# Kernel tuning notes

Measured on AMD Instinct MI355X. Metric: run time of the kernel, lower is better.

The kernel has to match this reference:

```python
import jax, jax.numpy as jnp
import numpy as np
import math

B, S, D, H = 2, 2048, 1024, 16
DH = D // H

def setup_inputs() -> dict:
    key = jax.random.key(0)
    ks = jax.random.split(key, 12)
    s = 1.0 / math.sqrt(D)
    return {
        "q": jax.random.normal(ks[0], (B, S, D), jnp.float32),
        "k": jax.random.normal(ks[1], (B, S, D), jnp.float32),
        "v": jax.random.normal(ks[2], (B, S, D), jnp.float32),
        "mask": jnp.tril(jnp.ones((S, S), dtype=bool)),  # causal mask
        "Wq": jax.random.normal(ks[3], (D, D), jnp.float32) * s,
        "bq": jnp.zeros((D,), jnp.float32),
        "Wk": jax.random.normal(ks[4], (D, D), jnp.float32) * s,
        "bk": jnp.zeros((D,), jnp.float32),
        "Wv": jax.random.normal(ks[5], (D, D), jnp.float32) * s,
        "bv": jnp.zeros((D,), jnp.float32),
        "Wo": jax.random.normal(ks[6], (D, D), jnp.float32) * s,
        "bo": jnp.zeros((D,), jnp.float32),
    }

def _split_heads(x):
    b, s, _ = x.shape
    return x.reshape(b, s, H, DH).transpose(0, 2, 1, 3)  # [B,H,S,DH]

def reference(q, k, v, mask, Wq, bq, Wk, bk, Wv, bv, Wo, bo):
    qh = _split_heads(q @ Wq.T + bq)
    kh = _split_heads(k @ Wk.T + bk)
    vh = _split_heads(v @ Wv.T + bv)
    scale = 1.0 / math.sqrt(DH)
    scores = jnp.einsum('bhqd,bhkd->bhqk', qh, kh) * scale  # [B,H,S,S]
    scores = jnp.where(mask[None, None, :, :], scores, -jnp.inf)
    attn = jax.nn.softmax(scores, axis=-1)
    out = jnp.einsum('bhqk,bhkd->bhqd', attn, vh)  # [B,H,S,DH]
    out = out.transpose(0, 2, 1, 3).reshape(B, S, D)  # combine heads
    return out @ Wo.T + bo
```

## Files before the change

### kernel.cpp

```cpp
#include <hip/hip_runtime.h>

typedef unsigned int u32;
typedef unsigned short u16;
typedef __attribute__((ext_vector_type(8))) short bf16x8;
typedef __attribute__((ext_vector_type(8))) u16 u16x8;
typedef __attribute__((ext_vector_type(4))) u16 u16x4;
typedef __attribute__((ext_vector_type(4))) float f32x4;
typedef __attribute__((ext_vector_type(2))) u32 u32x2;

#define AS1 __attribute__((address_space(1)))
#define AS3 __attribute__((address_space(3)))

__device__ __forceinline__ void gload_lds16(const void* g, void* l) {
  __builtin_amdgcn_global_load_lds((const AS1 u32*)g, (AS3 u32*)l, 16, 0, 0);
}

__device__ __forceinline__ u16 f2bf(float f) {
  union { float f; u32 u; } x; x.f = f;
  u32 u = x.u;
  return (u16)((u + 0x7fffu + ((u >> 16) & 1u)) >> 16);
}

__device__ __forceinline__ float bf2f(u16 v) {
  union { u32 u; float f; } x; x.u = (u32)v << 16; return x.f;
}

__device__ __forceinline__ u32 cvt_pk_bf16(float lo, float hi) {
  u32 r;
  asm("v_cvt_pk_bf16_f32 %0, %1, %2" : "=v"(r) : "v"(lo), "v"(hi));
  return r;
}

__device__ __forceinline__ float fexp2(float x) {
  float r;
  asm("v_exp_f32 %0, %1" : "=v"(r) : "v"(x));
  return r;
}

__global__ __launch_bounds__(256) void convert_w(
    const float* __restrict__ wq, const float* __restrict__ wk,
    const float* __restrict__ wv, const float* __restrict__ wo,
    u16* __restrict__ dst)
{
  int b = blockIdx.x, t = threadIdx.x;
  int w = b >> 9;
  const float* sp = (w == 0) ? wq : ((w == 1) ? wk : ((w == 2) ? wv : wo));
  size_t lb = (size_t)(b & 511) * 2048 + (size_t)t * 8;
  f32x4 f0 = *(const f32x4*)(sp + lb);
  f32x4 f1 = *(const f32x4*)(sp + lb + 4);
  u16x8 o;
  o[0]=f2bf(f0[0]); o[1]=f2bf(f0[1]); o[2]=f2bf(f0[2]); o[3]=f2bf(f0[3]);
  o[4]=f2bf(f1[0]); o[5]=f2bf(f1[1]); o[6]=f2bf(f1[2]); o[7]=f2bf(f1[3]);
  *(u16x8*)(dst + (size_t)b*2048 + (size_t)t*8) = o;
}

__global__ __launch_bounds__(256, 3) void gemm_qkv(
    const float* __restrict__ Xq, const float* __restrict__ Xk, const float* __restrict__ Xv,
    const u16* __restrict__ Wall,
    const float* __restrict__ bq, const float* __restrict__ bk, const float* __restrict__ bv,
    u16* __restrict__ Cqk, u16* __restrict__ VT)
{
  __shared__ __align__(16) u16 lds[24576];
  const int t = threadIdx.x;
  const int wid = t >> 6, l = t & 63;
  const int c = l & 15, g = l >> 4;
  const int u = blockIdx.x;
  const int lid = (u & 7) * 96 + (u >> 3);
  const int which = lid >> 8;
  const int r5 = lid & 255;
  const int m0 = (r5 >> 3) * 128, n0 = (r5 & 7) * 128;
  const float* Afp = (which == 0) ? Xq : ((which == 1) ? Xk : Xv);
  const u16* Bw = Wall + (size_t)which * 1048576;
  const int wr = wid >> 1, wc = wid & 1;

  const int srow = wid*16 + (l >> 2);
  const int gch = ((l & 3) ^ (srow & 3) ^ ((srow >> 2) & 3)) << 3;
  const float* Ag0 = Afp + (size_t)(m0 + srow)*1024      + gch;
  const float* Ag1 = Afp + (size_t)(m0 + 64 + srow)*1024 + gch;
  const int awr0 = wid*512 + l*8;
  const int awr1 = 2048 + wid*512 + l*8;
  const u16* Bsrc0 = Bw + (size_t)(n0 + srow)*1024      + gch;
  const u16* Bsrc1 = Bw + (size_t)(n0 + 64 + srow)*1024 + gch;
  const int wbase = wid * 512;

  f32x4 ra0, ra1, ra2, ra3;

#define A_LOAD(j) do { \
    const float* ap0_ = Ag0 + ((j) << 5); \
    const float* ap1_ = Ag1 + ((j) << 5); \
    ra0 = *(const f32x4*)ap0_; ra1 = *(const f32x4*)(ap0_ + 4); \
    ra2 = *(const f32x4*)ap1_; ra3 = *(const f32x4*)(ap1_ + 4); \
  } while (0)

#define A_CVT_WRITE(j) do { \
    const int bo_ = ((j) % 3) * 8192; \
    u16x8 w0_, w1_; u32* q0_ = (u32*)&w0_; u32* q1_ = (u32*)&w1_; \
    q0_[0]=cvt_pk_bf16(ra0[0],ra0[1]); q0_[1]=cvt_pk_bf16(ra0[2],ra0[3]); \
    q0_[2]=cvt_pk_bf16(ra1[0],ra1[1]); q0_[3]=cvt_pk_bf16(ra1[2],ra1[3]); \
    q1_[0]=cvt_pk_bf16(ra2[0],ra2[1]); q1_[1]=cvt_pk_bf16(ra2[2],ra2[3]); \
    q1_[2]=cvt_pk_bf16(ra3[0],ra3[1]); q1_[3]=cvt_pk_bf16(ra3[2],ra3[3]); \
    *(u16x8*)&lds[bo_ + awr0] = w0_; \
    *(u16x8*)&lds[bo_ + awr1] = w1_; \
  } while (0)

#define B_STAGE(j) do { \
    const int bo_ = ((j) % 3) * 8192; const int ko_ = (j) << 5; \
    gload_lds16(Bsrc0 + ko_, &lds[bo_ + 4096 + wbase]); \
    gload_lds16(Bsrc1 + ko_, &lds[bo_ + 6144 + wbase]); \
  } while (0)

  const int fswz = (g ^ (c & 3) ^ ((c >> 2) & 3)) << 3;
  const int abase = (wr*64 + c)*32 + fswz;
  const int bbase = 4096 + (wc*64 + c)*32 + fswz;

  f32x4 acc[4][4] = {};

  A_LOAD(0);
  B_STAGE(0);
  B_STAGE(1);
  asm volatile("s_waitcnt vmcnt(2)" ::: "memory");
  A_CVT_WRITE(0);
  A_LOAD(1);
  asm volatile("s_waitcnt lgkmcnt(0)" ::: "memory");
  __builtin_amdgcn_s_barrier();
  __builtin_amdgcn_sched_barrier(0);

#pragma unroll
  for (int tstep = 0; tstep < 32; ++tstep) {
    if (tstep + 2 < 32) B_STAGE(tstep + 2);
    const int bo = (tstep % 3) * 8192;
    bf16x8 af[4], bf[4];
#pragma unroll
    for (int mf = 0; mf < 4; ++mf)
      af[mf] = *(const bf16x8*)&lds[bo + abase + mf*512];
#pragma unroll
    for (int nf = 0; nf < 4; ++nf)
      bf[nf] = *(const bf16x8*)&lds[bo + bbase + nf*512];
    __builtin_amdgcn_s_setprio(1);
#pragma unroll
    for (int mf = 0; mf < 4; ++mf)
#pragma unroll
      for (int nf = 0; nf < 4; ++nf)
        acc[mf][nf] = __builtin_amdgcn_mfma_f32_16x16x32_bf16(af[mf], bf[nf], acc[mf][nf], 0, 0, 0);
    __builtin_amdgcn_s_setprio(0);
    if (tstep + 1 < 32) {
      if (tstep + 2 < 32) asm volatile("s_waitcnt vmcnt(2)" ::: "memory");
      else                asm volatile("s_waitcnt vmcnt(0)" ::: "memory");
      A_CVT_WRITE(tstep + 1);
      if (tstep + 2 < 32) A_LOAD(tstep + 2);
    }
    asm volatile("s_waitcnt lgkmcnt(0)" ::: "memory");
    __builtin_amdgcn_s_barrier();
    __builtin_amdgcn_sched_barrier(0);
  }
#undef A_LOAD
#undef A_CVT_WRITE
#undef B_STAGE

  const float* bias = (which == 0) ? bq : ((which == 1) ? bk : bv);
  if (which < 2) {
#pragma unroll
    for (int mf = 0; mf < 4; ++mf)
#pragma unroll
      for (int nf = 0; nf < 4; ++nf) {
        int row = m0 + wr*64 + mf*16 + g*4;
        int col = n0 + wc*64 + nf*16 + c;
        float bv_ = bias[col];
        int colg = which*1024 + col;
#pragma unroll
        for (int r = 0; r < 4; ++r)
          Cqk[(size_t)(row+r)*2048 + colg] = f2bf(acc[mf][nf][r] + bv_);
      }
  } else {
#pragma unroll
    for (int mf = 0; mf < 4; ++mf)
#pragma unroll
      for (int nf = 0; nf < 4; ++nf) {
        int row = m0 + wr*64 + mf*16 + g*4;
        int col = n0 + wc*64 + nf*16 + c;
        float bv_ = bias[col];
        int bb2 = row >> 11, s = row & 2047;
        int hh = col >> 6, dh = col & 63;
        u16x4 pk;
#pragma unroll
        for (int r = 0; r < 4; ++r) pk[r] = f2bf(acc[mf][nf][r] + bv_);
        *(u16x4*)&VT[((size_t)(((bb2<<4)+hh)<<6) + dh)*2048 + s] = pk;
      }
  }
}

__global__ __launch_bounds__(256, 3) void gemm_out(
    const u16* __restrict__ A, const u16* __restrict__ Bw,
    const float* __restrict__ bias, float* __restrict__ C)
{
  __shared__ __align__(16) u16 lds[24576];
  const int t = threadIdx.x;
  const int wid = t >> 6, l = t & 63;
  const int c = l & 15, g = l >> 4;
  const int u = blockIdx.x;
  const int lid = (u & 7) * 32 + (u >> 3);
  const int m0 = (lid >> 3) * 128, n0 = (lid & 7) * 128;
  const int wr = wid >> 1, wc = wid & 1;

  const int srow = wid*16 + (l >> 2);
  const int sswz = (((l & 3) ^ (srow & 3) ^ ((srow >> 2) & 3)) << 3);
  const u16* Asrc0 = A  + (size_t)(m0 + srow)*1024      + sswz;
  const u16* Asrc1 = A  + (size_t)(m0 + 64 + srow)*1024 + sswz;
  const u16* Bsrc0 = Bw + (size_t)(n0 + srow)*1024      + sswz;
  const u16* Bsrc1 = Bw + (size_t)(n0 + 64 + srow)*1024 + sswz;
  const int wbase = wid * 512;

#define O_STAGE(j) do { \
    const int bo_ = ((j) % 3) * 8192; const int ko_ = (j) << 5; \
    gload_lds16(Asrc0 + ko_, &lds[bo_ + wbase]); \
    gload_lds16(Asrc1 + ko_, &lds[bo_ + 2048 + wbase]); \
    gload_lds16(Bsrc0 + ko_, &lds[bo_ + 4096 + wbase]); \
    gload_lds16(Bsrc1 + ko_, &lds[bo_ + 6144 + wbase]); \
  } while (0)

  const int fswz = (g ^ (c & 3) ^ ((c >> 2) & 3)) << 3;
  const int abase = (wr*64 + c)*32 + fswz;
  const int bbase = 4096 + (wc*64 + c)*32 + fswz;

  f32x4 acc[4][4] = {};

  O_STAGE(0);
  O_STAGE(1);
  asm volatile("s_waitcnt vmcnt(4)" ::: "memory");
  __builtin_amdgcn_s_barrier();
  __builtin_amdgcn_sched_barrier(0);

#pragma unroll
  for (int tstep = 0; tstep < 32; ++tstep) {
    if (tstep + 2 < 32) O_STAGE(tstep + 2);
    const int bo = (tstep % 3) * 8192;
    bf16x8 af[4], bf[4];
#pragma unroll
    for (int mf = 0; mf < 4; ++mf)
      af[mf] = *(const bf16x8*)&lds[bo + abase + mf*512];
#pragma unroll
    for (int nf = 0; nf < 4; ++nf)
      bf[nf] = *(const bf16x8*)&lds[bo + bbase + nf*512];
    __builtin_amdgcn_s_setprio(1);
#pragma unroll
    for (int mf = 0; mf < 4; ++mf)
#pragma unroll
      for (int nf = 0; nf < 4; ++nf)
        acc[mf][nf] = __builtin_amdgcn_mfma_f32_16x16x32_bf16(af[mf], bf[nf], acc[mf][nf], 0, 0, 0);
    __builtin_amdgcn_s_setprio(0);
    if (tstep + 2 < 32) asm volatile("s_waitcnt vmcnt(4)" ::: "memory");
    else                asm volatile("s_waitcnt vmcnt(0)" ::: "memory");
    __builtin_amdgcn_s_barrier();
    __builtin_amdgcn_sched_barrier(0);
  }
#undef O_STAGE

#pragma unroll
  for (int mf = 0; mf < 4; ++mf)
#pragma unroll
    for (int nf = 0; nf < 4; ++nf) {
      int row = m0 + wr*64 + mf*16 + g*4;
      int col = n0 + wc*64 + nf*16 + c;
      float bv_ = bias[col];
#pragma unroll
      for (int r = 0; r < 4; ++r)
        C[(size_t)(row+r)*1024 + col] = acc[mf][nf][r] + bv_;
    }
}

__device__ __forceinline__ void stage_kv(u16* lds, const u16* Kt, const u16* Vt,
                                         int buf, int wid) {
#pragma unroll
  for (int ii = 0; ii < 2; ++ii)
    gload_lds16(Kt + (size_t)ii*32*2048, &lds[4096 + buf*4096 + ii*2048 + wid*512]);
#pragma unroll
  for (int ii = 0; ii < 2; ++ii)
    gload_lds16(Vt + (size_t)ii*32*2048, &lds[12288 + buf*4096 + ii*2048 + wid*512]);
}

__device__ __forceinline__ void attn_phase(
    u16* lds, const u16* Qg, const u16* Ka, const u16* Va,
    int q0, int kt0, int nkv, bool maskLast,
    int wid, int g, int c, int arow, int achk, int pbase, int cs,
    float& MI, float& LI, f32x4 (&o)[4])
{
  const float SC = 0.18033688f;
#pragma unroll
  for (int i = 0; i < 2; ++i) {
    int row = i*32 + arow;
    gload_lds16(Qg + (size_t)(q0+row)*2048 + ((achk ^ (row&7)) << 3),
                &lds[i*2048 + wid*512]);
  }
  const u16* Kt = Ka + (size_t)kt0 * (64*2048);
  const u16* Vt = Va + kt0 * 64;
  stage_kv(lds, Kt, Vt, 0, wid);
  asm volatile("s_waitcnt vmcnt(0)" ::: "memory");
  __builtin_amdgcn_s_barrier();
  __builtin_amdgcn_sched_barrier(0);

  bf16x8 qf[2];
#pragma unroll
  for (int kh = 0; kh < 2; ++kh) {
    int row = wid*16 + c;
    int ch = (kh*4 + g) ^ (row & 7);
    qf[kh] = *(const bf16x8*)&lds[row*64 + ch*8];
  }

  float mi = -INFINITY, li = 0.f;
#pragma unroll
  for (int df = 0; df < 4; ++df) o[df] = f32x4{0.f, 0.f, 0.f, 0.f};

  for (int i = 0; i < nkv; ++i) {
    if (i + 1 < nkv) {
      Kt += 64*2048; Vt += 64;
      stage_kv(lds, Kt, Vt, (i+1)&1, wid);
    }
    const u16* Kb = &lds[4096  + (i&1)*4096];
    const u16* Vb = &lds[12288 + (i&1)*4096];

    f32x4 sT[4] = {};
    __builtin_amdgcn_s_setprio(1);
#pragma unroll
    for (int kh = 0; kh < 2; ++kh) {
      bf16x8 kf[4];
#pragma unroll
      for (int nf = 0; nf < 4; ++nf) {
        int row = nf*16 + c;
        int ch = (kh*4 + g) ^ (c & 7);
        kf[nf] = *(const bf16x8*)&Kb[row*64 + ch*8];
      }
#pragma unroll
      for (int nf = 0; nf < 4; ++nf)
        sT[nf] = __builtin_amdgcn_mfma_f32_16x16x32_bf16(kf[nf], qf[kh], sT[nf], 0,0,0);
    }
    __builtin_amdgcn_s_setprio(0);

    if (maskLast && i == nkv - 1) {
#pragma unroll
      for (int nf = 0; nf < 4; ++nf)
#pragma unroll
        for (int r = 0; r < 4; ++r)
          if (nf*16 + g*4 + r > wid*16 + c) sT[nf][r] = -INFINITY;
    }

    float mx = fmaxf(fmaxf(sT[0][0], sT[0][1]), fmaxf(sT[0][2], sT[0][3]));
#pragma unroll
    for (int nf = 1; nf < 4; ++nf)
      mx = fmaxf(mx, fmaxf(fmaxf(sT[nf][0], sT[nf][1]), fmaxf(sT[nf][2], sT[nf][3])));
    if (!__all(mx * SC <= mi + 8.f)) {
      float mxr = fmaxf(mx, __shfl_xor(mx, 16, 64));
      mxr = fmaxf(mxr, __shfl_xor(mxr, 32, 64));
      float mn = fmaxf(mi, mxr * SC);
      float corr = fexp2(mi - mn);
      li *= corr;
#pragma unroll
      for (int df = 0; df < 4; ++df) {
        o[df][0] *= corr; o[df][1] *= corr;
        o[df][2] *= corr; o[df][3] *= corr;
      }
      mi = mn;
    }
    float sum = 0.f;
#pragma unroll
    for (int nf = 0; nf < 4; ++nf)
#pragma unroll
      for (int r = 0; r < 4; ++r) {
        float pv = fexp2(fmaf(sT[nf][r], SC, -mi));
        sT[nf][r] = pv;
        sum += pv;
      }
    li += sum;

#pragma unroll
    for (int nf = 0; nf < 4; ++nf) {
      u32x2 ww;
      ww[0] = cvt_pk_bf16(sT[nf][0], sT[nf][1]);
      ww[1] = cvt_pk_bf16(sT[nf][2], sT[nf][3]);
      int ch = (2*nf + (g >> 1)) ^ cs;
      *(u32x2*)&lds[pbase + c*64 + ch*8 + (g & 1)*4] = ww;
    }
    asm volatile("s_waitcnt lgkmcnt(0)" ::: "memory");
    __builtin_amdgcn_sched_barrier(0);

    __builtin_amdgcn_s_setprio(1);
#pragma unroll
    for (int kh = 0; kh < 2; ++kh) {
      bf16x8 pfr, vf[4];
      {
        int ch = (kh*4 + g) ^ cs;
        pfr = *(const bf16x8*)&lds[pbase + c*64 + ch*8];
      }
#pragma unroll
      for (int df = 0; df < 4; ++df) {
        int d = df*16 + c;
        int ch = (kh*4 + g) ^ (d & 7);
        vf[df] = *(const bf16x8*)&Vb[d*64 + ch*8];
      }
#pragma unroll
      for (int df = 0; df < 4; ++df)
        o[df] = __builtin_amdgcn_mfma_f32_16x16x32_bf16(vf[df], pfr, o[df], 0,0,0);
    }
    __builtin_amdgcn_s_setprio(0);

    asm volatile("s_waitcnt vmcnt(0)" ::: "memory");
    __builtin_amdgcn_s_barrier();
    __builtin_amdgcn_sched_barrier(0);
  }
  MI = mi; LI = li;
}

__device__ __forceinline__ void store_partial(
    u16* __restrict__ part, int slot, int s,
    int wid, int g, int c, float mi, float li_tot, const f32x4 (&o)[4])
{
  u16* po = part + (size_t)(slot*2 + s) * 4608;
  int q = wid*16 + c;
#pragma unroll
  for (int df = 0; df < 4; ++df) {
    u16x4 pk;
    pk[0] = f2bf(o[df][0]); pk[1] = f2bf(o[df][1]);
    pk[2] = f2bf(o[df][2]); pk[3] = f2bf(o[df][3]);
    *(u16x4*)&po[q*64 + df*16 + g*4] = pk;
  }
  if (g == 0) {
    ((float*)(po + 4096))[q] = mi;
    ((float*)(po + 4224))[q] = li_tot;
  }
}

__global__ __launch_bounds__(256, 4) void attn_fwd(
    const u16* __restrict__ QK, const u16* __restrict__ VT,
    u16* __restrict__ AO, u16* __restrict__ part)
{
  __shared__ __align__(16) u16 lds[20480];
  const int t = threadIdx.x;
  const int wid = t >> 6, l = t & 63;
  const int g = l >> 4, c = l & 15;
  const int u = blockIdx.x;
  const int lid = (u & 7) * 128 + (u >> 3);
  const int gx = lid & 31, h = (lid >> 5) & 15, b = lid >> 9;
  const int p = gx >> 1, s = gx & 1;
  const u16* Qg  = QK + (size_t)b * 2048 * 2048 + (size_t)h * 64;
  const u16* Kg  = Qg + 1024;
  const u16* VTg = VT + (size_t)(((b << 4) + h) << 6) * 2048;
  const int arow = t >> 3, achk = t & 7;
  const int pbase = wid * 1024;
  const int cs = (c & 7) ^ ((c >> 3) << 2);
  const u16* Ka = Kg  + (size_t)arow*2048 + ((achk ^ (arow & 7)) << 3);
  const u16* Va = VTg + (size_t)arow*2048 + ((achk ^ (arow & 7)) << 3);
  const int slot = ((b*16 + h)*16 + p);

  float mi, li; f32x4 o[4];

  if (s == 0) {
    attn_phase(lds, Qg, Ka, Va, p*64, 0, p+1, true,
               wid, g, c, arow, achk, pbase, cs, mi, li, o);
    {
      float lt = li + __shfl_xor(li, 16, 64);
      lt += __shfl_xor(lt, 32, 64);
      float nr = 1.f / lt;
      int row = p*64 + wid*16 + c;
      size_t rb = ((size_t)b*2048 + row)*1024 + h*64;
#pragma unroll
      for (int df = 0; df < 4; ++df) {
        u16x4 pk;
        pk[0] = f2bf(o[df][0] * nr); pk[1] = f2bf(o[df][1] * nr);
        pk[2] = f2bf(o[df][2] * nr); pk[3] = f2bf(o[df][3] * nr);
        *(u16x4*)&AO[rb + df*16 + g*4] = pk;
      }
    }
    attn_phase(lds, Qg, Ka, Va, (31-p)*64, 0, 16-p, false,
               wid, g, c, arow, achk, pbase, cs, mi, li, o);
    float lt = li + __shfl_xor(li, 16, 64);
    lt += __shfl_xor(lt, 32, 64);
    store_partial(part, slot, 0, wid, g, c, mi, lt, o);
  } else {
    attn_phase(lds, Qg, Ka, Va, (31-p)*64, 16-p, 16, true,
               wid, g, c, arow, achk, pbase, cs, mi, li, o);
    float lt = li + __shfl_xor(li, 16, 64);
    lt += __shfl_xor(lt, 32, 64);
    store_partial(part, slot, 1, wid, g, c, mi, lt, o);
  }
}

__global__ __launch_bounds__(256) void attn_merge(
    const u16* __restrict__ part, u16* __restrict__ AO)
{
  int slot = blockIdx.x;
  int p = slot & 15;
  int h = (slot >> 4) & 15;
  int b = slot >> 8;
  const u16* p0 = part + (size_t)slot * 9216;
  const u16* p1 = p0 + 4608;
  int t = threadIdx.x;
  int r = t >> 2, c0 = (t & 3) * 16;
  float m0 = ((const float*)(p0 + 4096))[r], m1 = ((const float*)(p1 + 4096))[r];
  float l0 = ((const float*)(p0 + 4224))[r], l1 = ((const float*)(p1 + 4224))[r];
  float m = fmaxf(m0, m1);
  float e0 = exp2f(m0 - m), e1 = exp2f(m1 - m);
  float rl = 1.f / (l0*e0 + l1*e1);
  e0 *= rl; e1 *= rl;
  const u16x8* a0 = (const u16x8*)(p0 + r*64 + c0);
  const u16x8* a1 = (const u16x8*)(p1 + r*64 + c0);
  int qrow = (31 - p)*64 + r;
  size_t ab = ((size_t)b*2048 + qrow)*1024 + h*64 + c0;
#pragma unroll
  for (int half = 0; half < 2; ++half) {
    u16x8 x = a0[half], y = a1[half];
    u16x8 w;
#pragma unroll
    for (int j = 0; j < 8; ++j)
      w[j] = f2bf(bf2f(x[j])*e0 + bf2f(y[j])*e1);
    *(u16x8*)&AO[ab + half*8] = w;
  }
}

extern "C" void kernel_launch(void* const* d_in, const int* in_sizes, int n_in,
                              void* d_out, int out_size, void* d_ws, size_t ws_size,
                              hipStream_t stream)
{
  const float* q  = (const float*)d_in[0];
  const float* k  = (const float*)d_in[1];
  const float* v  = (const float*)d_in[2];
  const float* Wq = (const float*)d_in[4];
  const float* bq = (const float*)d_in[5];
  const float* Wk = (const float*)d_in[6];
  const float* bk = (const float*)d_in[7];
  const float* Wv = (const float*)d_in[8];
  const float* bv = (const float*)d_in[9];
  const float* Wo = (const float*)d_in[10];
  const float* bo = (const float*)d_in[11];
  float* out = (float*)d_out;

  u16* ws   = (u16*)d_ws;
  u16* Wqb  = ws + 12582912;
  u16* Wob  = ws + 15728640;
  u16* QKp  = ws + 16777216;
  u16* VTp  = ws + 25165824;
  u16* AO   = ws + 29360128;

  convert_w<<<2048, 256, 0, stream>>>(Wq, Wk, Wv, Wo, Wqb);

  gemm_qkv<<<768, 256, 0, stream>>>(q, k, v, Wqb, bq, bk, bv, QKp, VTp);

  attn_fwd<<<1024, 256, 0, stream>>>(QKp, VTp, AO, ws);

  attn_merge<<<512, 256, 0, stream>>>(ws, AO);

  gemm_out<<<256, 256, 0, stream>>>(AO, Wob, bo, out);
}
```

Before: 101.3 us.

## Double attention query tile to 128 rows per block, two 16-row fragments per wave

Each attention block now handles 128 query rows instead of 64, and each wave computes two 16-row MFMA fragments that share the same K and V fragments loaded from LDS. This halves the K/V global-to-LDS traffic per unit of work and the LDS reads per MFMA. In exchange, register use and the LDS footprint grow, occupancy is lowered to 2 blocks per CU, the grid halves to 512 blocks, and the causal mask now spans the last two KV tiles. The partial-result layout and the merge kernel are resized to match.

```diff
diff --git a/kernel.cpp b/kernel.cpp
--- a/kernel.cpp
+++ b/kernel.cpp
@@ -272,21 +272,21 @@
                                          int buf, int wid) {
 #pragma unroll
   for (int ii = 0; ii < 2; ++ii)
-    gload_lds16(Kt + (size_t)ii*32*2048, &lds[4096 + buf*4096 + ii*2048 + wid*512]);
+    gload_lds16(Kt + (size_t)ii*32*2048, &lds[8192  + buf*4096 + ii*2048 + wid*512]);
 #pragma unroll
   for (int ii = 0; ii < 2; ++ii)
-    gload_lds16(Vt + (size_t)ii*32*2048, &lds[12288 + buf*4096 + ii*2048 + wid*512]);
+    gload_lds16(Vt + (size_t)ii*32*2048, &lds[16384 + buf*4096 + ii*2048 + wid*512]);
 }
 
 __device__ __forceinline__ void attn_phase(
     u16* lds, const u16* Qg, const u16* Ka, const u16* Va,
-    int q0, int kt0, int nkv, bool maskLast,
+    int q0, int kt0, int nkv, bool maskTail,
     int wid, int g, int c, int arow, int achk, int pbase, int cs,
-    float& MI, float& LI, f32x4 (&o)[4])
+    float (&mi)[2], float (&li)[2], f32x4 (&o)[2][4])
 {
   const float SC = 0.18033688f;
 #pragma unroll
-  for (int i = 0; i < 2; ++i) {
+  for (int i = 0; i < 4; ++i) {
     int row = i*32 + arow;
     gload_lds16(Qg + (size_t)(q0+row)*2048 + ((achk ^ (row&7)) << 3),
                 &lds[i*2048 + wid*512]);
@@ -298,27 +298,34 @@
   __builtin_amdgcn_s_barrier();
   __builtin_amdgcn_sched_barrier(0);
 
-  bf16x8 qf[2];
-#pragma unroll
-  for (int kh = 0; kh < 2; ++kh) {
-    int row = wid*16 + c;
-    int ch = (kh*4 + g) ^ (row & 7);
-    qf[kh] = *(const bf16x8*)&lds[row*64 + ch*8];
-  }
-
-  float mi = -INFINITY, li = 0.f;
-#pragma unroll
-  for (int df = 0; df < 4; ++df) o[df] = f32x4{0.f, 0.f, 0.f, 0.f};
+  bf16x8 qf[2][2];
+#pragma unroll
+  for (int mf = 0; mf < 2; ++mf)
+#pragma unroll
+    for (int kh = 0; kh < 2; ++kh) {
+      int row = wid*32 + mf*16 + c;
+      int ch = (kh*4 + g) ^ (c & 7);
+      qf[mf][kh] = *(const bf16x8*)&lds[row*64 + ch*8];
+    }
+  __builtin_amdgcn_s_barrier();
+
+#pragma unroll
+  for (int mf = 0; mf < 2; ++mf) {
+    mi[mf] = -INFINITY; li[mf] = 0.f;
+#pragma unroll
+    for (int df = 0; df < 4; ++df) o[mf][df] = f32x4{0.f, 0.f, 0.f, 0.f};
+  }
+  const int qb0 = q0 + wid*32;
 
   for (int i = 0; i < nkv; ++i) {
     if (i + 1 < nkv) {
       Kt += 64*2048; Vt += 64;
       stage_kv(lds, Kt, Vt, (i+1)&1, wid);
     }
-    const u16* Kb = &lds[4096  + (i&1)*4096];
-    const u16* Vb = &lds[12288 + (i&1)*4096];
-
-    f32x4 sT[4] = {};
+    const u16* Kb = &lds[8192  + (i&1)*4096];
+    const u16* Vb = &lds[16384 + (i&1)*4096];
+
+    f32x4 sT[2][4] = {};
     __builtin_amdgcn_s_setprio(1);
 #pragma unroll
     for (int kh = 0; kh < 2; ++kh) {
@@ -330,54 +337,62 @@
         kf[nf] = *(const bf16x8*)&Kb[row*64 + ch*8];
       }
 #pragma unroll
+      for (int mf = 0; mf < 2; ++mf)
+#pragma unroll
+        for (int nf = 0; nf < 4; ++nf)
+          sT[mf][nf] = __builtin_amdgcn_mfma_f32_16x16x32_bf16(kf[nf], qf[mf][kh], sT[mf][nf], 0,0,0);
+    }
+    __builtin_amdgcn_s_setprio(0);
+
+    if (maskTail && i >= nkv - 2) {
+      const int k0g = (kt0 + i) * 64;
+#pragma unroll
+      for (int mf = 0; mf < 2; ++mf)
+#pragma unroll
+        for (int nf = 0; nf < 4; ++nf)
+#pragma unroll
+          for (int r = 0; r < 4; ++r)
+            if (k0g + nf*16 + g*4 + r > qb0 + mf*16 + c) sT[mf][nf][r] = -INFINITY;
+    }
+
+#pragma unroll
+    for (int mf = 0; mf < 2; ++mf) {
+      float mx = fmaxf(fmaxf(sT[mf][0][0], sT[mf][0][1]), fmaxf(sT[mf][0][2], sT[mf][0][3]));
+#pragma unroll
+      for (int nf = 1; nf < 4; ++nf)
+        mx = fmaxf(mx, fmaxf(fmaxf(sT[mf][nf][0], sT[mf][nf][1]), fmaxf(sT[mf][nf][2], sT[mf][nf][3])));
+      if (!__all(mx * SC <= mi[mf] + 8.f)) {
+        float mxr = fmaxf(mx, __shfl_xor(mx, 16, 64));
+        mxr = fmaxf(mxr, __shfl_xor(mxr, 32, 64));
+        float mn = fmaxf(mi[mf], mxr * SC);
+        float corr = fexp2(mi[mf] - mn);
+        li[mf] *= corr;
+#pragma unroll
+        for (int df = 0; df < 4; ++df) {
+          o[mf][df][0] *= corr; o[mf][df][1] *= corr;
+          o[mf][df][2] *= corr; o[mf][df][3] *= corr;
+        }
+        mi[mf] = mn;
+      }
+      float sum = 0.f;
+#pragma unroll
       for (int nf = 0; nf < 4; ++nf)
-        sT[nf] = __builtin_amdgcn_mfma_f32_16x16x32_bf16(kf[nf], qf[kh], sT[nf], 0,0,0);
-    }
-    __builtin_amdgcn_s_setprio(0);
-
-    if (maskLast && i == nkv - 1) {
-#pragma unroll
-      for (int nf = 0; nf < 4; ++nf)
-#pragma unroll
-        for (int r = 0; r < 4; ++r)
-          if (nf*16 + g*4 + r > wid*16 + c) sT[nf][r] = -INFINITY;
-    }
-
-    float mx = fmaxf(fmaxf(sT[0][0], sT[0][1]), fmaxf(sT[0][2], sT[0][3]));
-#pragma unroll
-    for (int nf = 1; nf < 4; ++nf)
-      mx = fmaxf(mx, fmaxf(fmaxf(sT[nf][0], sT[nf][1]), fmaxf(sT[nf][2], sT[nf][3])));
-    if (!__all(mx * SC <= mi + 8.f)) {
-      float mxr = fmaxf(mx, __shfl_xor(mx, 16, 64));
-      mxr = fmaxf(mxr, __shfl_xor(mxr, 32, 64));
-      float mn = fmaxf(mi, mxr * SC);
-      float corr = fexp2(mi - mn);
-      li *= corr;
-#pragma unroll
-      for (int df = 0; df < 4; ++df) {
-        o[df][0] *= corr; o[df][1] *= corr;
-        o[df][2] *= corr; o[df][3] *= corr;
-      }
-      mi = mn;
-    }
-    float sum = 0.f;
-#pragma unroll
-    for (int nf = 0; nf < 4; ++nf)
-#pragma unroll
-      for (int r = 0; r < 4; ++r) {
-        float pv = fexp2(fmaf(sT[nf][r], SC, -mi));
-        sT[nf][r] = pv;
-        sum += pv;
-      }
-    li += sum;
-
-#pragma unroll
-    for (int nf = 0; nf < 4; ++nf) {
-      u32x2 ww;
-      ww[0] = cvt_pk_bf16(sT[nf][0], sT[nf][1]);
-      ww[1] = cvt_pk_bf16(sT[nf][2], sT[nf][3]);
-      int ch = (2*nf + (g >> 1)) ^ cs;
-      *(u32x2*)&lds[pbase + c*64 + ch*8 + (g & 1)*4] = ww;
+#pragma unroll
+        for (int r = 0; r < 4; ++r) {
+          float pv = fexp2(fmaf(sT[mf][nf][r], SC, -mi[mf]));
+          sT[mf][nf][r] = pv;
+          sum += pv;
+        }
+      li[mf] += sum;
+
+#pragma unroll
+      for (int nf = 0; nf < 4; ++nf) {
+        u32x2 ww;
+        ww[0] = cvt_pk_bf16(sT[mf][nf][0], sT[mf][nf][1]);
+        ww[1] = cvt_pk_bf16(sT[mf][nf][2], sT[mf][nf][3]);
+        int ch = (2*nf + (g >> 1)) ^ cs;
+        *(u32x2*)&lds[pbase + mf*1024 + c*64 + ch*8 + (g & 1)*4] = ww;
+      }
     }
     asm volatile("s_waitcnt lgkmcnt(0)" ::: "memory");
     __builtin_amdgcn_sched_barrier(0);
@@ -385,10 +400,11 @@
     __builtin_amdgcn_s_setprio(1);
 #pragma unroll
     for (int kh = 0; kh < 2; ++kh) {
-      bf16x8 pfr, vf[4];
-      {
+      bf16x8 pfr[2], vf[4];
+#pragma unroll
+      for (int mf = 0; mf < 2; ++mf) {
         int ch = (kh*4 + g) ^ cs;
-        pfr = *(const bf16x8*)&lds[pbase + c*64 + ch*8];
+        pfr[mf] = *(const bf16x8*)&lds[pbase + mf*1024 + c*64 + ch*8];
       }
 #pragma unroll
       for (int df = 0; df < 4; ++df) {
@@ -397,8 +413,10 @@
         vf[df] = *(const bf16x8*)&Vb[d*64 + ch*8];
       }
 #pragma unroll
-      for (int df = 0; df < 4; ++df)
-        o[df] = __builtin_amdgcn_mfma_f32_16x16x32_bf16(vf[df], pfr, o[df], 0,0,0);
+      for (int mf = 0; mf < 2; ++mf)
+#pragma unroll
+        for (int df = 0; df < 4; ++df)
+          o[mf][df] = __builtin_amdgcn_mfma_f32_16x16x32_bf16(vf[df], pfr[mf], o[mf][df], 0,0,0);
     }
     __builtin_amdgcn_s_setprio(0);
 
@@ -406,79 +424,92 @@
     __builtin_amdgcn_s_barrier();
     __builtin_amdgcn_sched_barrier(0);
   }
-  MI = mi; LI = li;
 }
 
 __device__ __forceinline__ void store_partial(
     u16* __restrict__ part, int slot, int s,
-    int wid, int g, int c, float mi, float li_tot, const f32x4 (&o)[4])
-{
-  u16* po = part + (size_t)(slot*2 + s) * 4608;
-  int q = wid*16 + c;
-#pragma unroll
-  for (int df = 0; df < 4; ++df) {
-    u16x4 pk;
-    pk[0] = f2bf(o[df][0]); pk[1] = f2bf(o[df][1]);
-    pk[2] = f2bf(o[df][2]); pk[3] = f2bf(o[df][3]);
-    *(u16x4*)&po[q*64 + df*16 + g*4] = pk;
-  }
-  if (g == 0) {
-    ((float*)(po + 4096))[q] = mi;
-    ((float*)(po + 4224))[q] = li_tot;
-  }
-}
-
-__global__ __launch_bounds__(256, 4) void attn_fwd(
+    int wid, int g, int c, const float (&mi)[2], const float (&lt)[2],
+    const f32x4 (&o)[2][4])
+{
+  u16* po = part + (size_t)(slot*2 + s) * 8704;
+#pragma unroll
+  for (int mf = 0; mf < 2; ++mf) {
+    int q = wid*32 + mf*16 + c;
+#pragma unroll
+    for (int df = 0; df < 4; ++df) {
+      u16x4 pk;
+      pk[0] = f2bf(o[mf][df][0]); pk[1] = f2bf(o[mf][df][1]);
+      pk[2] = f2bf(o[mf][df][2]); pk[3] = f2bf(o[mf][df][3]);
+      *(u16x4*)&po[q*64 + df*16 + g*4] = pk;
+    }
+    if (g == 0) {
+      ((float*)(po + 8192))[q] = mi[mf];
+      ((float*)(po + 8448))[q] = lt[mf];
+    }
+  }
+}
+
+__global__ __launch_bounds__(256, 2) void attn_fwd(
     const u16* __restrict__ QK, const u16* __restrict__ VT,
     u16* __restrict__ AO, u16* __restrict__ part)
 {
-  __shared__ __align__(16) u16 lds[20480];
+  __shared__ __align__(16) u16 lds[24576];
   const int t = threadIdx.x;
   const int wid = t >> 6, l = t & 63;
   const int g = l >> 4, c = l & 15;
   const int u = blockIdx.x;
-  const int lid = (u & 7) * 128 + (u >> 3);
-  const int gx = lid & 31, h = (lid >> 5) & 15, b = lid >> 9;
+  const int lid = (u & 7) * 64 + (u >> 3);
+  const int gx = lid & 15, h = (lid >> 4) & 15, b = lid >> 8;
   const int p = gx >> 1, s = gx & 1;
   const u16* Qg  = QK + (size_t)b * 2048 * 2048 + (size_t)h * 64;
   const u16* Kg  = Qg + 1024;
   const u16* VTg = VT + (size_t)(((b << 4) + h) << 6) * 2048;
   const int arow = t >> 3, achk = t & 7;
-  const int pbase = wid * 1024;
+  const int pbase = wid * 2048;
   const int cs = (c & 7) ^ ((c >> 3) << 2);
   const u16* Ka = Kg  + (size_t)arow*2048 + ((achk ^ (arow & 7)) << 3);
   const u16* Va = VTg + (size_t)arow*2048 + ((achk ^ (arow & 7)) << 3);
-  const int slot = ((b*16 + h)*16 + p);
-
-  float mi, li; f32x4 o[4];
+  const int slot = ((b*16 + h)*8 + p);
+
+  float mi[2], li[2]; f32x4 o[2][4];
 
   if (s == 0) {
-    attn_phase(lds, Qg, Ka, Va, p*64, 0, p+1, true,
+    attn_phase(lds, Qg, Ka, Va, p*128, 0, 2*p+2, true,
                wid, g, c, arow, achk, pbase, cs, mi, li, o);
-    {
-      float lt = li + __shfl_xor(li, 16, 64);
+#pragma unroll
+    for (int mf = 0; mf < 2; ++mf) {
+      float lt = li[mf] + __shfl_xor(li[mf], 16, 64);
       lt += __shfl_xor(lt, 32, 64);
       float nr = 1.f / lt;
-      int row = p*64 + wid*16 + c;
+      int row = p*128 + wid*32 + mf*16 + c;
       size_t rb = ((size_t)b*2048 + row)*1024 + h*64;
 #pragma unroll
       for (int df = 0; df < 4; ++df) {
         u16x4 pk;
-        pk[0] = f2bf(o[df][0] * nr); pk[1] = f2bf(o[df][1] * nr);
-        pk[2] = f2bf(o[df][2] * nr); pk[3] = f2bf(o[df][3] * nr);
+        pk[0] = f2bf(o[mf][df][0] * nr); pk[1] = f2bf(o[mf][df][1] * nr);
+        pk[2] = f2bf(o[mf][df][2] * nr); pk[3] = f2bf(o[mf][df][3] * nr);
         *(u16x4*)&AO[rb + df*16 + g*4] = pk;
       }
     }
-    attn_phase(lds, Qg, Ka, Va, (31-p)*64, 0, 16-p, false,
+    __builtin_amdgcn_s_barrier();
+    attn_phase(lds, Qg, Ka, Va, (15-p)*128, 0, 15-2*p, false,
                wid, g, c, arow, achk, pbase, cs, mi, li, o);
-    float lt = li + __shfl_xor(li, 16, 64);
-    lt += __shfl_xor(lt, 32, 64);
+    float lt[2];
+#pragma unroll
+    for (int mf = 0; mf < 2; ++mf) {
+      lt[mf] = li[mf] + __shfl_xor(li[mf], 16, 64);
+      lt[mf] += __shfl_xor(lt[mf], 32, 64);
+    }
     store_partial(part, slot, 0, wid, g, c, mi, lt, o);
   } else {
-    attn_phase(lds, Qg, Ka, Va, (31-p)*64, 16-p, 16, true,
+    attn_phase(lds, Qg, Ka, Va, (15-p)*128, 15-2*p, 17, true,
                wid, g, c, arow, achk, pbase, cs, mi, li, o);
-    float lt = li + __shfl_xor(li, 16, 64);
-    lt += __shfl_xor(lt, 32, 64);
+    float lt[2];
+#pragma unroll
+    for (int mf = 0; mf < 2; ++mf) {
+      lt[mf] = li[mf] + __shfl_xor(li[mf], 16, 64);
+      lt[mf] += __shfl_xor(lt[mf], 32, 64);
+    }
     store_partial(part, slot, 1, wid, g, c, mi, lt, o);
   }
 }
@@ -487,31 +518,31 @@
     const u16* __restrict__ part, u16* __restrict__ AO)
 {
   int slot = blockIdx.x;
-  int p = slot & 15;
-  int h = (slot >> 4) & 15;
-  int b = slot >> 8;
-  const u16* p0 = part + (size_t)slot * 9216;
-  const u16* p1 = p0 + 4608;
+  int p = slot & 7;
+  int h = (slot >> 3) & 15;
+  int b = slot >> 7;
+  const u16* p0 = part + (size_t)slot * 17408;
+  const u16* p1 = p0 + 8704;
   int t = threadIdx.x;
-  int r = t >> 2, c0 = (t & 3) * 16;
-  float m0 = ((const float*)(p0 + 4096))[r], m1 = ((const float*)(p1 + 4096))[r];
-  float l0 = ((const float*)(p0 + 4224))[r], l1 = ((const float*)(p1 + 4224))[r];
+  int r = t >> 1, c0 = (t & 1) * 32;
+  float m0 = ((const float*)(p0 + 8192))[r], m1 = ((const float*)(p1 + 8192))[r];
+  float l0 = ((const float*)(p0 + 8448))[r], l1 = ((const float*)(p1 + 8448))[r];
   float m = fmaxf(m0, m1);
   float e0 = exp2f(m0 - m), e1 = exp2f(m1 - m);
   float rl = 1.f / (l0*e0 + l1*e1);
   e0 *= rl; e1 *= rl;
   const u16x8* a0 = (const u16x8*)(p0 + r*64 + c0);
   const u16x8* a1 = (const u16x8*)(p1 + r*64 + c0);
-  int qrow = (31 - p)*64 + r;
+  int qrow = (15 - p)*128 + r;
   size_t ab = ((size_t)b*2048 + qrow)*1024 + h*64 + c0;
 #pragma unroll
-  for (int half = 0; half < 2; ++half) {
-    u16x8 x = a0[half], y = a1[half];
+  for (int q8 = 0; q8 < 4; ++q8) {
+    u16x8 x = a0[q8], y = a1[q8];
     u16x8 w;
 #pragma unroll
     for (int j = 0; j < 8; ++j)
       w[j] = f2bf(bf2f(x[j])*e0 + bf2f(y[j])*e1);
-    *(u16x8*)&AO[ab + half*8] = w;
+    *(u16x8*)&AO[ab + q8*8] = w;
   }
 }
 
@@ -543,9 +574,9 @@
 
   gemm_qkv<<<768, 256, 0, stream>>>(q, k, v, Wqb, bq, bk, bv, QKp, VTp);
 
-  attn_fwd<<<1024, 256, 0, stream>>>(QKp, VTp, AO, ws);
-
-  attn_merge<<<512, 256, 0, stream>>>(ws, AO);
+  attn_fwd<<<512, 256, 0, stream>>>(QKp, VTp, AO, ws);
+
+  attn_merge<<<256, 256, 0, stream>>>(ws, AO);
 
   gemm_out<<<256, 256, 0, stream>>>(AO, Wob, bo, out);
 }
```

After: 100.4 us. Within noise of the previous version (-0.9%).
